# Performance work log

Measured on AMD Instinct MI355X. Metric: run time of the kernel, lower is better.

The kernel has to match this reference:

```python
import jax, jax.numpy as jnp
import numpy as np

B=64; HW=14; E=2048; L=30; V=10000; EMB=512; AML=768; ADL=500
D=512+ADL   # decoder_dim + article_downlen = 1012
A=512+ADL   # attention_dim + article_downlen = 1012

def setup_inputs() -> dict:
    key = jax.random.key(0)
    ks = jax.random.split(key, 20)
    s = 0.02
    lin = lambda k, i, o: (jax.random.normal(k, (i, o), jnp.float32) * s)
    inp = {}
    inp['encoder_out'] = jax.random.normal(ks[0], (B, HW, HW, E), jnp.float32)
    inp['encoded_captions'] = jax.random.randint(ks[1], (B, L), 0, V)
    cl = jax.random.randint(ks[2], (B, 1), 2, L + 1)
    inp['caption_lengths'] = cl.at[0, 0].set(L)  # ensure max decode length == L-1
    inp['encoded_articles'] = jax.random.normal(ks[3], (B, 1, AML), jnp.float32)
    inp['article_lengths'] = jax.random.randint(ks[4], (B, 1), 1, AML)
    inp['blank_context'] = 0
    inp['E_emb'] = jax.random.uniform(ks[5], (V, EMB), jnp.float32, -0.1, 0.1)
    inp['W_par'] = lin(ks[6], AML, ADL); inp['b_par'] = jnp.zeros(ADL, jnp.float32)
    inp['W_enc'] = lin(ks[7], E, A);     inp['b_enc'] = jnp.zeros(A, jnp.float32)
    inp['W_dec'] = lin(ks[8], D, A);     inp['b_dec'] = jnp.zeros(A, jnp.float32)
    inp['W_full'] = lin(ks[9], A, 1);    inp['b_full'] = jnp.zeros(1, jnp.float32)
    inp['W_h'] = lin(ks[10], E + ADL, D); inp['b_h'] = jnp.zeros(D, jnp.float32)
    inp['W_c'] = lin(ks[11], E + ADL, D); inp['b_c'] = jnp.zeros(D, jnp.float32)
    inp['W_fb'] = lin(ks[12], D, E);      inp['b_fb'] = jnp.zeros(E, jnp.float32)
    inp['W_ih'] = lin(ks[13], EMB + E, 4 * D); inp['b_ih'] = jnp.zeros(4 * D, jnp.float32)
    inp['W_hh'] = lin(ks[14], D, 4 * D);       inp['b_hh'] = jnp.zeros(4 * D, jnp.float32)
    inp['W_fc'] = jax.random.uniform(ks[15], (D, V), jnp.float32, -0.1, 0.1)
    inp['b_fc'] = jnp.zeros(V, jnp.float32)
    return inp

def reference(encoder_out, encoded_captions, caption_lengths, encoded_articles,
              article_lengths, blank_context, E_emb, W_par, b_par, W_enc, b_enc,
              W_dec, b_dec, W_full, b_full, W_h, b_h, W_c, b_c, W_fb, b_fb,
              W_ih, b_ih, W_hh, b_hh, W_fc, b_fc):
    Bv = encoder_out.shape[0]
    enc = encoder_out.reshape(Bv, -1, encoder_out.shape[-1])  # (B, P, E)
    lens = caption_lengths[:, 0]
    sort_ind = jnp.argsort(-lens)
    lens = lens[sort_ind]
    enc = enc[sort_ind]
    caps = encoded_captions[sort_ind]
    arts = encoded_articles[sort_ind]
    emb = E_emb[caps]                                   # (B, L, EMB)
    context = (arts @ W_par + b_par)[:, 0, :]           # ParagraphEncoder -> (B, ADL)
    dec_in = jnp.concatenate([enc.mean(axis=1), context], axis=1)
    h0 = dec_in @ W_h + b_h
    c0 = dec_in @ W_c + b_c
    dlens = lens - 1
    att1 = enc @ W_enc + b_enc                          # loop-invariant, (B, P, A)
    T = emb.shape[1] - 1

    def step(carry, t):
        h, c = carry
        active = (dlens > t)[:, None]                   # prefix mask (sorted desc)
        att2 = h @ W_dec + b_dec
        scores = (jax.nn.relu(att1 + att2[:, None, :]) @ W_full)[..., 0] + b_full[0]
        alpha = jax.nn.softmax(scores, axis=1)          # (B, P)
        awe = jnp.einsum('bp,bpe->be', alpha, enc)
        awe = jax.nn.sigmoid(h @ W_fb + b_fb) * awe     # gated attention encoding
        x = jnp.concatenate([emb[:, t, :], awe], axis=1)
        gates = x @ W_ih + b_ih + h @ W_hh + b_hh       # torch LSTMCell, gate order i,f,g,o
        i, f, g, o = jnp.split(gates, 4, axis=1)
        c_new = jax.nn.sigmoid(f) * c + jax.nn.sigmoid(i) * jnp.tanh(g)
        h_new = jax.nn.sigmoid(o) * jnp.tanh(c_new)
        preds = jnp.where(active, h_new @ W_fc + b_fc, 0.0)
        alpha_m = jnp.where(active, alpha, 0.0)
        h = jnp.where(active, h_new, h)
        c = jnp.where(active, c_new, c)
        return (h, c), (preds, alpha_m)

    _, (preds, alphas) = jax.lax.scan(step, (h0, c0), jnp.arange(T))
    predictions = jnp.transpose(preds, (1, 0, 2))       # (B, T, V)
    alphas = jnp.transpose(alphas, (1, 0, 2))           # (B, T, P)
    return (predictions, caps, dlens, alphas, sort_ind)
```

## Files before the change

kernel.cpp:

```cpp
#include <hip/hip_runtime.h>
#include <math.h>

#define B_   64
#define P_   196
#define E_   2048
#define L_   30
#define T_   29
#define V_   10000
#define EMB_ 512
#define AML_ 768
#define ADL_ 500
#define D_   1012
#define A_   1012
#define G4_  4048
#define XK_  2560

typedef unsigned short u16;
typedef __attribute__((ext_vector_type(8))) short bf16x8;
typedef __attribute__((ext_vector_type(4))) float f32x4;

__device__ __forceinline__ float sigf(float x) { return 1.f / (1.f + __expf(-x)); }
__device__ __forceinline__ float tanhf_fast(float x) { return 1.f - 2.f / (__expf(2.f * x) + 1.f); }
__device__ __forceinline__ u16 f2bf(float f) {
    unsigned u = __float_as_uint(f);
    return (u16)((u + 0x7FFFu + ((u >> 16) & 1u)) >> 16);
}
__device__ __forceinline__ float bf2f(u16 v) { return __uint_as_float(((unsigned)v) << 16); }

__global__ void k_setup(const int* __restrict__ clen, const int* __restrict__ caps,
                        float* __restrict__ out_caps, float* __restrict__ out_dlens,
                        float* __restrict__ out_sind,
                        int* __restrict__ sort_ind, int* __restrict__ dlens_i,
                        int* __restrict__ nact, int* __restrict__ caps_s)
{
    __shared__ int lens[B_];
    int t = threadIdx.x;
    if (t < B_) lens[t] = clen[t];
    __syncthreads();
    if (t < B_) {
        int my = lens[t];
        int rank = 0;
        for (int j = 0; j < B_; ++j) {
            int lj = lens[j];
            if (lj > my || (lj == my && j < t)) rank++;
        }
        sort_ind[rank] = t;
    }
    __syncthreads();
    if (t < B_) {
        int orig = sort_ind[t];
        int dl = lens[orig] - 1;
        dlens_i[t] = dl;
        out_dlens[t] = (float)dl;
        out_sind[t] = (float)orig;
        for (int j = 0; j < L_; ++j) {
            int cv = caps[orig * L_ + j];
            caps_s[t * L_ + j] = cv;
            out_caps[t * L_ + j] = (float)cv;
        }
    }
    __syncthreads();
    if (t < T_) {
        int cnt = 0;
        for (int j = 0; j < B_; ++j) cnt += (dlens_i[j] > t) ? 1 : 0;
        nact[t] = cnt;
    }
}

__global__ void k_zero(float4* __restrict__ p, long n4)
{
// ... 137 lines not shown
    const u16* w1p = W1 + (long)nc * K1 + lk;
    for (int k = 0; k < K1; k += 32) {
        bf16x8 bw = *(const bf16x8*)(w1p + k);
#pragma unroll
        for (int m = 0; m < 4; ++m)
            if (m < mmax) {
                bf16x8 aw = *(const bf16x8*)(a1p + (long)m * 16 * K1 + k);
                acc[m] = __builtin_amdgcn_mfma_f32_16x16x32_bf16(aw, bw, acc[m], 0, 0, 0);
            }
    }
    float bv = (n < Nmax) ? bias1[n] : 0.f;
#pragma unroll
    for (int m = 0; m < 4; ++m) {
        if (m < mmax) {
#pragma unroll
            for (int j = 0; j < 4; ++j) {
                int b = m * 16 + (lane >> 4) * 4 + j;
                if (b < Bact) {
                    float v = acc[m][j] + bv;
                    if (ACT == 1) v = sigf(v);
                    if (n < Nmax) {
                        if (OUT == 1) ((u16*)Yv)[(long)b * ldY + offY + n] = f2bf(v);
                        else          ((float*)Yv)[(long)b * ldY + offY + n] = v;
                    } else if (PADZ) {
                        if (OUT == 1) ((u16*)Yv)[(long)b * ldY + offY + n] = 0;
                        else          ((float*)Yv)[(long)b * ldY + offY + n] = 0.f;
                    }
                }
            }
        }
    }
}

__global__ void __launch_bounds__(256) k_att2fb(
    const u16* __restrict__ h_bf, const u16* __restrict__ WT_dec,
    const u16* __restrict__ WT_fb, const float* __restrict__ b_dec,
    const float* __restrict__ b_fb, float* __restrict__ att2p,
    float* __restrict__ fbp, const int* __restrict__ nact, int t)
{
    int Bact = nact[t];
    if (Bact <= 0) return;
    int mmax = (Bact + 15) >> 4;
    int kh = blockIdx.x >= 48;
    int nb = blockIdx.x - (kh ? 48 : 0);
    int isfb = nb >= 16;
    const u16* W = isfb ? WT_fb : WT_dec;
    const float* bias = isfb ? b_fb : b_dec;
    int Nmax = isfb ? E_ : A_;
    int nb2 = isfb ? nb - 16 : nb;
    long ldY = isfb ? (long)E_ : 1024L;
    float* Y = (isfb ? fbp : att2p) + (long)kh * B_ * ldY;

    int w = threadIdx.x >> 6, lane = threadIdx.x & 63;
    int lr = lane & 15, lk = (lane >> 4) * 8;
    int n = nb2 * 64 + w * 16 + lr;
    int nc = n < Nmax ? n : Nmax - 1;
    int k0 = kh * 512;
    f32x4 acc[4];
#pragma unroll
    for (int m = 0; m < 4; ++m) acc[m] = (f32x4){0.f, 0.f, 0.f, 0.f};
    const u16* ap = h_bf + (long)lr * 1024 + k0 + lk;
    const u16* wp = W + (long)nc * 1024 + k0 + lk;
    for (int k = 0; k < 512; k += 32) {
        bf16x8 bw = *(const bf16x8*)(wp + k);
#pragma unroll
        for (int m = 0; m < 4; ++m)
            if (m < mmax) {
                bf16x8 aw = *(const bf16x8*)(ap + (long)m * 16 * 1024 + k);
                acc[m] = __builtin_amdgcn_mfma_f32_16x16x32_bf16(aw, bw, acc[m], 0, 0, 0);
            }
    }
    if (n >= Nmax) return;
    float bv = (kh == 0) ? bias[n] : 0.f;
#pragma unroll
    for (int m = 0; m < 4; ++m) {
        if (m < mmax) {
#pragma unroll
            for (int j = 0; j < 4; ++j) {
                int b = m * 16 + (lane >> 4) * 4 + j;
                if (b < Bact) Y[(long)b * ldY + n] = acc[m][j] + bv;
            }
        }
    }
}

__global__ void k_scores(const u16* __restrict__ att1, const float* __restrict__ att2p,
                         const float* __restrict__ W_full, const float* __restrict__ b_full,
                         float* __restrict__ scores, const int* __restrict__ nact, int t)
{
    int b = blockIdx.y;
    if (b >= nact[t]) return;
    int wv = threadIdx.x >> 6;
    int lane = threadIdx.x & 63;
    int p = blockIdx.x * 4 + wv;
    const u16* a1 = att1 + ((long)b * P_ + p) * 1024;
    const float* a20 = att2p + (long)b * 1024;
    const float* a21 = att2p + (long)B_ * 1024 + (long)b * 1024;
    float acc = 0.f;
    for (int j2 = lane; j2 < 506; j2 += 64) {
        unsigned pk = *(const unsigned*)(a1 + 2 * j2);
        float2 p0 = *(const float2*)(a20 + 2 * j2);
        float2 p1 = *(const float2*)(a21 + 2 * j2);
        float2 wv2 = *(const float2*)(W_full + 2 * j2);
        float v0 = bf2f((u16)(pk & 0xFFFF)) + p0.x + p1.x;
        float v1 = bf2f((u16)(pk >> 16)) + p0.y + p1.y;
        v0 = v0 > 0.f ? v0 : 0.f;
        v1 = v1 > 0.f ? v1 : 0.f;
        acc = fmaf(v0, wv2.x, acc);
        acc = fmaf(v1, wv2.y, acc);
    }
    for (int m = 32; m >= 1; m >>= 1) acc += __shfl_xor(acc, m);
    if (lane == 0) scores[b * P_ + p] = acc + b_full[0];
}

__global__ void __launch_bounds__(256) k_awe_x(
    const u16* __restrict__ A_bf, const float* __restrict__ scores,
    const float* __restrict__ fbp, u16* __restrict__ awe_buf,
    float* __restrict__ alphas_out, const int* __restrict__ nact, int t)
{
    int b = blockIdx.y;
    if (b >= nact[t]) return;
    int tid = threadIdx.x;
    int w = tid >> 6, lane = tid & 63;
    __shared__ float al[P_];
    __shared__ float red[4];
    float v = (tid < P_) ? scores[b * P_ + tid] : -1e30f;
    float m = v;
    for (int s = 32; s >= 1; s >>= 1) m = fmaxf(m, __shfl_xor(m, s));
    if (lane == 0) red[w] = m;
    __syncthreads();
    m = fmaxf(fmaxf(red[0], red[1]), fmaxf(red[2], red[3]));
    float e = (tid < P_) ? __expf(v - m) : 0.f;
    float s_ = e;
    for (int s = 32; s >= 1; s >>= 1) s_ += __shfl_xor(s_, s);
    __syncthreads();
    if (lane == 0) red[w] = s_;
    __syncthreads();
    s_ = red[0] + red[1] + red[2] + red[3];
    if (tid < P_) al[tid] = e / s_;
    __syncthreads();

    if (blockIdx.x < 8) {
        int e0 = blockIdx.x * 256 + tid;
        const u16* src = A_bf + (long)b * P_ * E_ + e0;
        float s0 = 0.f, s1 = 0.f, s2 = 0.f, s3 = 0.f;
        for (int p = 0; p < P_; p += 4) {
            s0 = fmaf(al[p],     bf2f(src[(long)p * E_]), s0);
            s1 = fmaf(al[p + 1], bf2f(src[(long)(p + 1) * E_]), s1);
            s2 = fmaf(al[p + 2], bf2f(src[(long)(p + 2) * E_]), s2);
            s3 = fmaf(al[p + 3], bf2f(src[(long)(p + 3) * E_]), s3);
        }
        float g = sigf(fbp[(long)b * E_ + e0] + fbp[(long)(B_ + b) * E_ + e0]);
        awe_buf[(long)b * E_ + e0] = f2bf((s0 + s1 + s2 + s3) * g);
    } else {
        if (tid < P_) alphas_out[((long)b * T_ + t) * P_ + tid] = al[tid];
    }
}

__global__ void __launch_bounds__(256) k_gates(
    const u16* __restrict__ emb_t, const u16* __restrict__ awe,
    const u16* __restrict__ h_old, const u16* __restrict__ WT_ih,
    const u16* __restrict__ WT_hh, float* __restrict__ gpart,
    const int* __restrict__ nact, int t)
{
    int Bact = nact[t];
    if (Bact <= 0) return;
    int mmax = (Bact + 15) >> 4;
    int q = threadIdx.x >> 6;
    int lane = threadIdx.x & 63;
    int lr = lane & 15, lk = (lane >> 4) * 8;
    int kh = blockIdx.y;
    int n = blockIdx.x * 16 + lr;
    int nc = n < D_ ? n : D_ - 1;
    f32x4 acc[4];
#pragma unroll
    for (int m = 0; m < 4; ++m) acc[m] = (f32x4){0.f, 0.f, 0.f, 0.f};
    const u16* wih = WT_ih + ((long)q * D_ + nc) * XK_;
    const u16* whh = WT_hh + ((long)q * D_ + nc) * 1024;

    if (kh == 0) {
        const u16* ap = emb_t + (long)lr * EMB_ + lk;
        for (int k = 0; k < EMB_; k += 32) {
            bf16x8 bw = *(const bf16x8*)(wih + k);
#pragma unroll
            for (int m = 0; m < 4; ++m)
                if (m < mmax) {
                    bf16x8 aw = *(const bf16x8*)(ap + (long)m * 16 * EMB_ + k);
                    acc[m] = __builtin_amdgcn_mfma_f32_16x16x32_bf16(aw, bw, acc[m], 0, 0, 0);
                }
        }
        const u16* ap2 = awe + (long)lr * E_ + lk;
        const u16* w2 = wih + EMB_;
        for (int k = 0; k < 1280; k += 32) {
            bf16x8 bw = *(const bf16x8*)(w2 + k);
#pragma unroll
            for (int m = 0; m < 4; ++m)
                if (m < mmax) {
                    bf16x8 aw = *(const bf16x8*)(ap2 + (long)m * 16 * E_ + k);
                    acc[m] = __builtin_amdgcn_mfma_f32_16x16x32_bf16(aw, bw, acc[m], 0, 0, 0);
                }
        }
    } else {
        const u16* ap2 = awe + (long)lr * E_ + 1280 + lk;
        const u16* w2 = wih + 1792;
        for (int k = 0; k < 768; k += 32) {
            bf16x8 bw = *(const bf16x8*)(w2 + k);
#pragma unroll
            for (int m = 0; m < 4; ++m)
                if (m < mmax) {
                    bf16x8 aw = *(const bf16x8*)(ap2 + (long)m * 16 * E_ + k);
                    acc[m] = __builtin_amdgcn_mfma_f32_16x16x32_bf16(aw, bw, acc[m], 0, 0, 0);
                }
        }
        const u16* ap3 = h_old + (long)lr * 1024 + lk;
        for (int k = 0; k < 1024; k += 32) {
            bf16x8 bw = *(const bf16x8*)(whh + k);
#pragma unroll
            for (int m = 0; m < 4; ++m)
                if (m < mmax) {
                    bf16x8 aw = *(const bf16x8*)(ap3 + (long)m * 16 * 1024 + k);
                    acc[m] = __builtin_amdgcn_mfma_f32_16x16x32_bf16(aw, bw, acc[m], 0, 0, 0);
                }
        }
    }
#pragma unroll
    for (int m = 0; m < 4; ++m) {
        if (m < mmax) {
#pragma unroll
            for (int j = 0; j < 4; ++j) {
                int bb = m * 16 + (lane >> 4) * 4 + j;
                if (bb < Bact)
                    gpart[((long)kh * B_ + bb) * 4096 + q * 1024 + n] = acc[m][j];
            }
        }
    }
}

__global__ void k_lstm_red(const float* __restrict__ gpart, const float* __restrict__ b_ih,
                           const float* __restrict__ b_hh, float* __restrict__ cbuf,
                           u16* __restrict__ h_new, const int* __restrict__ nact, int t)
{
    int b = blockIdx.y;
    if (b >= nact[t]) return;
    int n = blockIdx.x * 256 + threadIdx.x;
    if (n >= D_) return;
    const float* g0 = gpart + (long)b * 4096;
    const float* g1 = gpart + (long)(B_ + b) * 4096;
    float gi = g0[n]        + g1[n]        + b_ih[n]          + b_hh[n];
    float gf = g0[1024 + n] + g1[1024 + n] + b_ih[D_ + n]     + b_hh[D_ + n];
    float gg = g0[2048 + n] + g1[2048 + n] + b_ih[2 * D_ + n] + b_hh[2 * D_ + n];
    float go = g0[3072 + n] + g1[3072 + n] + b_ih[3 * D_ + n] + b_hh[3 * D_ + n];
    float c = cbuf[(long)b * 1024 + n];
    float cn = sigf(gf) * c + sigf(gi) * tanhf_fast(gg);
    float hn = sigf(go) * tanhf_fast(cn);
    cbuf[(long)b * 1024 + n] = cn;
    h_new[(long)b * 1024 + n] = f2bf(hn);
}

__global__ void __launch_bounds__(256) k_fc_all(
    const u16* __restrict__ h_all, const u16* __restrict__ W,
    const float* __restrict__ bias, float* __restrict__ out_preds,
    const int* __restrict__ nact)
{
    int tslot = blockIdx.y;
    int Bact = nact[tslot];
    if (Bact <= 0) return;
    int mmax = (Bact + 15) >> 4;
    int w = threadIdx.x >> 6, lane = threadIdx.x & 63;
    int lr = lane & 15, lk = (lane >> 4) * 8;
    int n0 = blockIdx.x * 256 + w * 64;
    f32x4 acc[4][4];
#pragma unroll
    for (int i = 0; i < 4; ++i)
#pragma unroll
        for (int j = 0; j < 4; ++j) acc[i][j] = (f32x4){0.f, 0.f, 0.f, 0.f};
    const u16* ap = h_all + ((long)(tslot + 1) * B_ + lr) * 1024 + lk;
    int ncl[4];
#pragma unroll
    for (int nt = 0; nt < 4; ++nt) {
        int n = n0 + nt * 16 + lr;
        ncl[nt] = n < V_ ? n : V_ - 1;
    }
    for (int k = 0; k < 1024; k += 32) {
        bf16x8 af[4], bf[4];
#pragma unroll
        for (int mt = 0; mt < 4; ++mt)
            if (mt < mmax) af[mt] = *(const bf16x8*)(ap + (long)mt * 16 * 1024 + k);
#pragma unroll
        for (int nt = 0; nt < 4; ++nt) bf[nt] = *(const bf16x8*)(W + (long)ncl[nt] * 1024 + lk + k);
// ... 33 lines not shown
    const float* arts   = (const float*)d_in[3];
    const float* E_emb  = (const float*)d_in[6];
    const float* W_par  = (const float*)d_in[7];
    const float* b_par  = (const float*)d_in[8];
    const float* W_enc  = (const float*)d_in[9];
    const float* b_enc  = (const float*)d_in[10];
    const float* W_dec  = (const float*)d_in[11];
    const float* b_dec  = (const float*)d_in[12];
    const float* W_full = (const float*)d_in[13];
    const float* b_full = (const float*)d_in[14];
    const float* W_h    = (const float*)d_in[15];
    const float* b_h    = (const float*)d_in[16];
    const float* W_c    = (const float*)d_in[17];
    const float* b_c    = (const float*)d_in[18];
    const float* W_fb   = (const float*)d_in[19];
    const float* b_fb   = (const float*)d_in[20];
    const float* W_ih   = (const float*)d_in[21];
    const float* b_ih   = (const float*)d_in[22];
    const float* W_hh   = (const float*)d_in[23];
    const float* b_hh   = (const float*)d_in[24];
    const float* W_fc   = (const float*)d_in[25];
    const float* b_fc   = (const float*)d_in[26];

    float* out = (float*)d_out;
    float* out_preds  = out;
    float* out_caps   = out + (long)B_ * T_ * V_;
    float* out_dlens  = out_caps + B_ * L_;
    float* out_alphas = out_dlens + B_;
    float* out_sind   = out_alphas + (long)B_ * T_ * P_;

    float* ws = (float*)d_ws;
    long o = 0;
    auto alloc = [&](long n) { long r = o; o += (n + 63) & ~63L; return r; };
    long o_ints   = alloc(2176);
    long o_decin  = alloc((long)B_ * XK_ / 2);
    long o_hall   = alloc((long)(T_ + 1) * B_ * 1024 / 2);
    long o_emball = alloc((long)T_ * B_ * EMB_ / 2);
    long o_awe    = alloc((long)B_ * E_ / 2);
    long o_c      = alloc((long)B_ * 1024);
    long o_att2p  = alloc((long)2 * B_ * 1024);
    long o_fbp    = alloc((long)2 * B_ * E_);
    long o_gpart  = alloc((long)2 * B_ * 4096);
    long o_scores = alloc((long)B_ * P_);
    long o_Abf    = alloc((long)12544 * E_ / 2);
    long o_att1   = alloc((long)12544 * 1024 / 2);
    long o_wtenc  = alloc((long)1024 * 2048 / 2);
    long o_wtdec  = alloc((long)1024 * 1024 / 2);
    long o_wtfb   = alloc((long)2048 * 1024 / 2);
    long o_wtih   = alloc((long)4096 * 2560 / 2);
    long o_wthh   = alloc((long)4096 * 1024 / 2);
    long o_wtfc   = alloc((long)10048 * 1024 / 2);

    int* sort_ind = (int*)(ws + o_ints);
    int* dlens_i  = sort_ind + 64;
    int* nact     = dlens_i + 64;
    int* caps_s   = nact + 32;
    u16*   dec_in  = (u16*)(ws + o_decin);
    u16*   h_all   = (u16*)(ws + o_hall);
    u16*   emb_all = (u16*)(ws + o_emball);
    u16*   awe_buf = (u16*)(ws + o_awe);
    float* cbuf   = ws + o_c;
    float* att2p  = ws + o_att2p;
    float* fbp    = ws + o_fbp;
    float* gpart  = ws + o_gpart;
    float* scores = ws + o_scores;
    u16*   A_bf   = (u16*)(ws + o_Abf);
    u16*   att1   = (u16*)(ws + o_att1);
    u16*   WT_enc = (u16*)(ws + o_wtenc);
    u16*   WT_dec = (u16*)(ws + o_wtdec);
    u16*   WT_fb  = (u16*)(ws + o_wtfb);
    u16*   WT_ih  = (u16*)(ws + o_wtih);
    u16*   WT_hh  = (u16*)(ws + o_wthh);
    u16*   WT_fc  = (u16*)(ws + o_wtfc);
    u16*   WT_h   = att1;
    u16*   WT_c   = att1 + (long)1024 * XK_;

    long n4 = ((long)B_ * T_ * V_ + B_ * L_ + B_ + (long)B_ * T_ * P_ + B_) / 4;
    k_zero<<<dim3((unsigned)((n4 + 255) / 256)), 256, 0, stream>>>((float4*)d_out, n4);
    k_setup<<<1, 64, 0, stream>>>(clen, caps, out_caps, out_dlens, out_sind,
                                  sort_ind, dlens_i, nact, caps_s);

    k_encmean<<<dim3(8, 64), 256, 0, stream>>>(enc, sort_ind, dec_in);
    k_ctx<<<dim3(2, 64), 256, 0, stream>>>(arts, W_par, b_par, sort_ind, dec_in);
    k_emb_all<<<dim3(T_, 64), 256, 0, stream>>>(E_emb, caps_s, emb_all);

    dim3 tb(32, 8);
    k_transpose<<<dim3(1024/32, 2560/32), tb, 0, stream>>>(W_h, WT_h, 2548, 1012, 2560, 1024);
    k_transpose<<<dim3(1024/32, 2560/32), tb, 0, stream>>>(W_c, WT_c, 2548, 1012, 2560, 1024);
    k_skinny<0,1,1><<<dim3(16), 256, 0, stream>>>(dec_in, WT_h, XK_, b_h, h_all, 1024L, 0L, D_,
                                                  nact, -1);
    k_skinny<0,0,1><<<dim3(16), 256, 0, stream>>>(dec_in, WT_c, XK_, b_c, cbuf, 1024L, 0L, D_,
                                                  nact, -1);

    k_transpose<<<dim3(1024/32, 2048/32), tb, 0, stream>>>(W_enc, WT_enc, 2048, 1012, 2048, 1024);
    k_transpose<<<dim3(1024/32, 1024/32), tb, 0, stream>>>(W_dec, WT_dec, 1012, 1012, 1024, 1024);
    k_transpose<<<dim3(2048/32, 1024/32), tb, 0, stream>>>(W_fb, WT_fb, 1012, 2048, 1024, 2048);
    k_transpose<<<dim3(4096/32, 2560/32), tb, 0, stream>>>(W_ih, WT_ih, 2560, 4048, 2560, 4096);
    k_transpose<<<dim3(4096/32, 1024/32), tb, 0, stream>>>(W_hh, WT_hh, 1012, 4048, 1024, 4096);
    k_transpose<<<dim3(10048/32, 1024/32), tb, 0, stream>>>(W_fc, WT_fc, 1012, 10000, 1024, 10048);

    k_cvt_enc<<<dim3(2, 12544), 256, 0, stream>>>(enc, sort_ind, A_bf);
    k_att1_mfma<<<dim3(4, 196), 256, 0, stream>>>(A_bf, WT_enc, b_enc, att1);

    for (int t = 0; t < T_; ++t) {
        const u16* h_old = h_all + (long)t * B_ * 1024;
        u16* h_new = h_all + (long)(t + 1) * B_ * 1024;
        const u16* emb_t = emb_all + (long)t * B_ * EMB_;
        k_att2fb<<<dim3(96), 256, 0, stream>>>(h_old, WT_dec, WT_fb, b_dec, b_fb,
                                               att2p, fbp, nact, t);
        k_scores<<<dim3(49, 64), 256, 0, stream>>>(att1, att2p, W_full, b_full, scores, nact, t);
        k_awe_x<<<dim3(9, 64), 256, 0, stream>>>(A_bf, scores, fbp, awe_buf,
                                                 out_alphas, nact, t);
        k_gates<<<dim3(64, 2), 256, 0, stream>>>(emb_t, awe_buf, h_old, WT_ih, WT_hh,
                                                 gpart, nact, t);
        k_lstm_red<<<dim3(4, 64), 256, 0, stream>>>(gpart, b_ih, b_hh, cbuf, h_new, nact, t);
    }
    k_fc_all<<<dim3(40, T_), 256, 0, stream>>>(h_all, WT_fc, b_fc, out_preds, nact);
}
```

Measured before the change: 3.111 ms.

## Fuse per-timestep decoder kernels into one persistent cooperative kernel with grid syncs

Replaces the five kernel launches per timestep (145 total) with a single cooperative kernel of 256 blocks that loops over timesteps and separates the phases with grid.sync. The h@W_hh product moves into the first phase alongside att2/fb, so it no longer sits on the critical path after the attention work. The input-to-hidden gates are split four ways across K to give more blocks work. This removes launch overhead and inter-kernel gaps, at the cost of grid-wide barriers and a fixed grid of 256 blocks that limits parallelism in the scores and awe phases.

New measurement: 7.037 ms. 2.26x slower.

```diff
diff --git a/kernel.cpp b/kernel.cpp
--- a/kernel.cpp
+++ b/kernel.cpp
@@ -1,5 +1,8 @@
 #include <hip/hip_runtime.h>
+#include <hip/hip_cooperative_groups.h>
 #include <math.h>
+
+namespace cg = cooperative_groups;
 
 #define B_   64
 #define P_   196
@@ -239,229 +242,212 @@
     }
 }
 
-__global__ void __launch_bounds__(256) k_att2fb(
-    const u16* __restrict__ h_bf, const u16* __restrict__ WT_dec,
-    const u16* __restrict__ WT_fb, const float* __restrict__ b_dec,
-    const float* __restrict__ b_fb, float* __restrict__ att2p,
-    float* __restrict__ fbp, const int* __restrict__ nact, int t)
-{
-    int Bact = nact[t];
-    if (Bact <= 0) return;
-    int mmax = (Bact + 15) >> 4;
-    int kh = blockIdx.x >= 48;
-    int nb = blockIdx.x - (kh ? 48 : 0);
-    int isfb = nb >= 16;
-    const u16* W = isfb ? WT_fb : WT_dec;
-    const float* bias = isfb ? b_fb : b_dec;
-    int Nmax = isfb ? E_ : A_;
-    int nb2 = isfb ? nb - 16 : nb;
-    long ldY = isfb ? (long)E_ : 1024L;
-    float* Y = (isfb ? fbp : att2p) + (long)kh * B_ * ldY;
-
-    int w = threadIdx.x >> 6, lane = threadIdx.x & 63;
-    int lr = lane & 15, lk = (lane >> 4) * 8;
-    int n = nb2 * 64 + w * 16 + lr;
-    int nc = n < Nmax ? n : Nmax - 1;
-    int k0 = kh * 512;
-    f32x4 acc[4];
-#pragma unroll
-    for (int m = 0; m < 4; ++m) acc[m] = (f32x4){0.f, 0.f, 0.f, 0.f};
-    const u16* ap = h_bf + (long)lr * 1024 + k0 + lk;
-    const u16* wp = W + (long)nc * 1024 + k0 + lk;
-    for (int k = 0; k < 512; k += 32) {
-        bf16x8 bw = *(const bf16x8*)(wp + k);
-#pragma unroll
-        for (int m = 0; m < 4; ++m)
-            if (m < mmax) {
-                bf16x8 aw = *(const bf16x8*)(ap + (long)m * 16 * 1024 + k);
-                acc[m] = __builtin_amdgcn_mfma_f32_16x16x32_bf16(aw, bw, acc[m], 0, 0, 0);
-            }
-    }
-    if (n >= Nmax) return;
-    float bv = (kh == 0) ? bias[n] : 0.f;
-#pragma unroll
-    for (int m = 0; m < 4; ++m) {
-        if (m < mmax) {
-#pragma unroll
-            for (int j = 0; j < 4; ++j) {
-                int b = m * 16 + (lane >> 4) * 4 + j;
-                if (b < Bact) Y[(long)b * ldY + n] = acc[m][j] + bv;
-            }
-        }
-    }
-}
-
-__global__ void k_scores(const u16* __restrict__ att1, const float* __restrict__ att2p,
-                         const float* __restrict__ W_full, const float* __restrict__ b_full,
-                         float* __restrict__ scores, const int* __restrict__ nact, int t)
-{
-    int b = blockIdx.y;
-    if (b >= nact[t]) return;
-    int wv = threadIdx.x >> 6;
-    int lane = threadIdx.x & 63;
-    int p = blockIdx.x * 4 + wv;
-    const u16* a1 = att1 + ((long)b * P_ + p) * 1024;
-    const float* a20 = att2p + (long)b * 1024;
-    const float* a21 = att2p + (long)B_ * 1024 + (long)b * 1024;
-    float acc = 0.f;
-    for (int j2 = lane; j2 < 506; j2 += 64) {
-        unsigned pk = *(const unsigned*)(a1 + 2 * j2);
-        float2 p0 = *(const float2*)(a20 + 2 * j2);
-        float2 p1 = *(const float2*)(a21 + 2 * j2);
-        float2 wv2 = *(const float2*)(W_full + 2 * j2);
-        float v0 = bf2f((u16)(pk & 0xFFFF)) + p0.x + p1.x;
-        float v1 = bf2f((u16)(pk >> 16)) + p0.y + p1.y;
-        v0 = v0 > 0.f ? v0 : 0.f;
-        v1 = v1 > 0.f ? v1 : 0.f;
-        acc = fmaf(v0, wv2.x, acc);
-        acc = fmaf(v1, wv2.y, acc);
-    }
-    for (int m = 32; m >= 1; m >>= 1) acc += __shfl_xor(acc, m);
-    if (lane == 0) scores[b * P_ + p] = acc + b_full[0];
-}
-
-__global__ void __launch_bounds__(256) k_awe_x(
-    const u16* __restrict__ A_bf, const float* __restrict__ scores,
-    const float* __restrict__ fbp, u16* __restrict__ awe_buf,
-    float* __restrict__ alphas_out, const int* __restrict__ nact, int t)
-{
-    int b = blockIdx.y;
-    if (b >= nact[t]) return;
+__global__ void __launch_bounds__(256) k_loop(
+    const u16* __restrict__ A_bf, const u16* __restrict__ att1,
+    const u16* __restrict__ emb_all,
+    const u16* __restrict__ WT_dec, const u16* __restrict__ WT_fb,
+    const u16* __restrict__ WT_hh, const u16* __restrict__ WT_ih,
+    const float* __restrict__ W_full, const float* __restrict__ b_full,
+    const float* __restrict__ b_dec, const float* __restrict__ b_fb,
+    const float* __restrict__ b_ih, const float* __restrict__ b_hh,
+    u16* __restrict__ h_all, float* __restrict__ cbuf,
+    float* __restrict__ att2p, float* __restrict__ fbp, float* __restrict__ ghp,
+    float* __restrict__ gpart, float* __restrict__ scores,
+    u16* __restrict__ awe_buf, float* __restrict__ alphas_out,
+    const int* __restrict__ nact)
+{
+    cg::grid_group grid = cg::this_grid();
+    int bid = blockIdx.x;
     int tid = threadIdx.x;
     int w = tid >> 6, lane = tid & 63;
+    int lr = lane & 15, lk = (lane >> 4) * 8;
     __shared__ float al[P_];
     __shared__ float red[4];
-    float v = (tid < P_) ? scores[b * P_ + tid] : -1e30f;
-    float m = v;
-    for (int s = 32; s >= 1; s >>= 1) m = fmaxf(m, __shfl_xor(m, s));
-    if (lane == 0) red[w] = m;
-    __syncthreads();
-    m = fmaxf(fmaxf(red[0], red[1]), fmaxf(red[2], red[3]));
-    float e = (tid < P_) ? __expf(v - m) : 0.f;
-    float s_ = e;
-    for (int s = 32; s >= 1; s >>= 1) s_ += __shfl_xor(s_, s);
-    __syncthreads();
-    if (lane == 0) red[w] = s_;
-    __syncthreads();
-    s_ = red[0] + red[1] + red[2] + red[3];
-    if (tid < P_) al[tid] = e / s_;
-    __syncthreads();
-
-    if (blockIdx.x < 8) {
-        int e0 = blockIdx.x * 256 + tid;
-        const u16* src = A_bf + (long)b * P_ * E_ + e0;
-        float s0 = 0.f, s1 = 0.f, s2 = 0.f, s3 = 0.f;
-        for (int p = 0; p < P_; p += 4) {
-            s0 = fmaf(al[p],     bf2f(src[(long)p * E_]), s0);
-            s1 = fmaf(al[p + 1], bf2f(src[(long)(p + 1) * E_]), s1);
-            s2 = fmaf(al[p + 2], bf2f(src[(long)(p + 2) * E_]), s2);
-            s3 = fmaf(al[p + 3], bf2f(src[(long)(p + 3) * E_]), s3);
-        }
-        float g = sigf(fbp[(long)b * E_ + e0] + fbp[(long)(B_ + b) * E_ + e0]);
-        awe_buf[(long)b * E_ + e0] = f2bf((s0 + s1 + s2 + s3) * g);
-    } else {
-        if (tid < P_) alphas_out[((long)b * T_ + t) * P_ + tid] = al[tid];
-    }
-}
-
-__global__ void __launch_bounds__(256) k_gates(
-    const u16* __restrict__ emb_t, const u16* __restrict__ awe,
-    const u16* __restrict__ h_old, const u16* __restrict__ WT_ih,
-    const u16* __restrict__ WT_hh, float* __restrict__ gpart,
-    const int* __restrict__ nact, int t)
-{
-    int Bact = nact[t];
-    if (Bact <= 0) return;
-    int mmax = (Bact + 15) >> 4;
-    int q = threadIdx.x >> 6;
-    int lane = threadIdx.x & 63;
-    int lr = lane & 15, lk = (lane >> 4) * 8;
-    int kh = blockIdx.y;
-    int n = blockIdx.x * 16 + lr;
-    int nc = n < D_ ? n : D_ - 1;
-    f32x4 acc[4];
-#pragma unroll
-    for (int m = 0; m < 4; ++m) acc[m] = (f32x4){0.f, 0.f, 0.f, 0.f};
-    const u16* wih = WT_ih + ((long)q * D_ + nc) * XK_;
-    const u16* whh = WT_hh + ((long)q * D_ + nc) * 1024;
-
-    if (kh == 0) {
-        const u16* ap = emb_t + (long)lr * EMB_ + lk;
-        for (int k = 0; k < EMB_; k += 32) {
-            bf16x8 bw = *(const bf16x8*)(wih + k);
-#pragma unroll
-            for (int m = 0; m < 4; ++m)
+
+    for (int t = 0; t < T_; ++t) {
+        int Bact = nact[t];
+        int mmax = (Bact + 15) >> 4;
+        const u16* h_old = h_all + (long)t * B_ * 1024;
+        u16* h_new = h_all + (long)(t + 1) * B_ * 1024;
+        const u16* emb_t = emb_all + (long)t * B_ * EMB_;
+
+        if (bid < 224) {
+            int u = bid, mode, kh, nloc0;
+            const u16* Wb; float* Y; long ldY;
+            if (u < 32)      { mode = 0; kh = u >> 4; nloc0 = (u & 15) * 64; Wb = WT_dec; Y = att2p + (long)kh * 65536;  ldY = 1024; }
+            else if (u < 96) { u -= 32; mode = 1; kh = u >> 5; nloc0 = (u & 31) * 64; Wb = WT_fb; Y = fbp + (long)kh * 131072; ldY = 2048; }
+            else             { u -= 96; mode = 2; kh = u >> 6; nloc0 = (u & 63) * 64; Wb = WT_hh; Y = ghp + (long)kh * 262144; ldY = 4096; }
+            int nloc = nloc0 + w * 16 + lr;
+            int wrow;
+            if (mode == 0)      wrow = nloc < A_ ? nloc : A_ - 1;
+            else if (mode == 1) wrow = nloc;
+            else { int q = nloc >> 10, d = nloc & 1023; wrow = q * D_ + (d < D_ ? d : D_ - 1); }
+            int k0 = kh * 512;
+            f32x4 acc[4];
+#pragma unroll
+            for (int m = 0; m < 4; ++m) acc[m] = (f32x4){0.f, 0.f, 0.f, 0.f};
+            const u16* ap = h_old + (long)lr * 1024 + k0 + lk;
+            const u16* wp = Wb + (long)wrow * 1024 + k0 + lk;
+            for (int k = 0; k < 512; k += 32) {
+                bf16x8 bw = *(const bf16x8*)(wp + k);
+#pragma unroll
+                for (int m = 0; m < 4; ++m)
+                    if (m < mmax) {
+                        bf16x8 aw = *(const bf16x8*)(ap + (long)m * 16 * 1024 + k);
+                        acc[m] = __builtin_amdgcn_mfma_f32_16x16x32_bf16(aw, bw, acc[m], 0, 0, 0);
+                    }
+            }
+            float bv = 0.f;
+            if (kh == 0) {
+                if (mode == 0) bv = (nloc < A_) ? b_dec[nloc] : 0.f;
+                else if (mode == 1) bv = b_fb[nloc];
+            }
+#pragma unroll
+            for (int m = 0; m < 4; ++m) {
                 if (m < mmax) {
-                    bf16x8 aw = *(const bf16x8*)(ap + (long)m * 16 * EMB_ + k);
-                    acc[m] = __builtin_amdgcn_mfma_f32_16x16x32_bf16(aw, bw, acc[m], 0, 0, 0);
+#pragma unroll
+                    for (int j = 0; j < 4; ++j) {
+                        int bb = m * 16 + (lane >> 4) * 4 + j;
+                        if (bb < Bact) Y[(long)bb * ldY + nloc] = acc[m][j] + bv;
+                    }
                 }
-        }
-        const u16* ap2 = awe + (long)lr * E_ + lk;
-        const u16* w2 = wih + EMB_;
-        for (int k = 0; k < 1280; k += 32) {
-            bf16x8 bw = *(const bf16x8*)(w2 + k);
-#pragma unroll
-            for (int m = 0; m < 4; ++m)
+            }
+        }
+        grid.sync();
+
+        {
+            int wave_id = bid * 4 + w;
+            float bf0 = b_full[0];
+            for (int pair = wave_id; pair < B_ * P_; pair += 1024) {
+                int b = pair / P_, p = pair - b * P_;
+                if (b >= Bact) continue;
+                const u16* a1 = att1 + ((long)b * P_ + p) * 1024;
+                const float* a20 = att2p + (long)b * 1024;
+                const float* a21 = att2p + 65536 + (long)b * 1024;
+                float acc = 0.f;
+                for (int j2 = lane; j2 < 506; j2 += 64) {
+                    unsigned pk = *(const unsigned*)(a1 + 2 * j2);
+                    float2 p0 = *(const float2*)(a20 + 2 * j2);
+                    float2 p1 = *(const float2*)(a21 + 2 * j2);
+                    float2 wv2 = *(const float2*)(W_full + 2 * j2);
+                    float v0 = bf2f((u16)(pk & 0xFFFF)) + p0.x + p1.x;
+                    float v1 = bf2f((u16)(pk >> 16)) + p0.y + p1.y;
+                    v0 = v0 > 0.f ? v0 : 0.f;
+                    v1 = v1 > 0.f ? v1 : 0.f;
+                    acc = fmaf(v0, wv2.x, acc);
+                    acc = fmaf(v1, wv2.y, acc);
+                }
+                for (int m = 32; m >= 1; m >>= 1) acc += __shfl_xor(acc, m);
+                if (lane == 0) scores[b * P_ + p] = acc + bf0;
+            }
+        }
+        grid.sync();
+
+        {
+            int b = bid & 63;
+            if (b < Bact) {
+                float v = (tid < P_) ? scores[b * P_ + tid] : -1e30f;
+                float m = v;
+                for (int s = 32; s >= 1; s >>= 1) m = fmaxf(m, __shfl_xor(m, s));
+                if (lane == 0) red[w] = m;
+                __syncthreads();
+                m = fmaxf(fmaxf(red[0], red[1]), fmaxf(red[2], red[3]));
+                float e = (tid < P_) ? __expf(v - m) : 0.f;
+                float s_ = e;
+                for (int s = 32; s >= 1; s >>= 1) s_ += __shfl_xor(s_, s);
+                __syncthreads();
+                if (lane == 0) red[w] = s_;
+                __syncthreads();
+                s_ = red[0] + red[1] + red[2] + red[3];
+                if (tid < P_) al[tid] = e / s_;
+                __syncthreads();
+
+                for (int part = bid >> 6; part < 9; part += 4) {
+                    if (part < 8) {
+                        int e0 = part * 256 + tid;
+                        const u16* src = A_bf + (long)b * P_ * E_ + e0;
+                        float s0 = 0.f, s1 = 0.f, s2 = 0.f, s3 = 0.f;
+                        for (int p = 0; p < P_; p += 4) {
+                            s0 = fmaf(al[p],     bf2f(src[(long)p * E_]), s0);
+                            s1 = fmaf(al[p + 1], bf2f(src[(long)(p + 1) * E_]), s1);
+                            s2 = fmaf(al[p + 2], bf2f(src[(long)(p + 2) * E_]), s2);
+                            s3 = fmaf(al[p + 3], bf2f(src[(long)(p + 3) * E_]), s3);
+                        }
+                        float g = sigf(fbp[(long)b * 2048 + e0] + fbp[131072 + (long)b * 2048 + e0]);
+                        awe_buf[(long)b * E_ + e0] = f2bf((s0 + s1 + s2 + s3) * g);
+                    } else {
+                        if (tid < P_) alphas_out[((long)b * T_ + t) * P_ + tid] = al[tid];
+                    }
+                }
+            }
+        }
+        grid.sync();
+
+        {
+            int nblk = bid & 63, kpart = bid >> 6;
+            int q = w;
+            int n = nblk * 16 + lr;
+            int nc = n < D_ ? n : D_ - 1;
+            const u16* wih = WT_ih + ((long)q * D_ + nc) * XK_;
+            f32x4 acc[4];
+#pragma unroll
+            for (int m = 0; m < 4; ++m) acc[m] = (f32x4){0.f, 0.f, 0.f, 0.f};
+            const u16* ap; long astr; const u16* wp; int K;
+            if (kpart == 0)      { ap = emb_t + (long)lr * EMB_ + lk;          astr = 16 * EMB_; wp = wih;        K = 512; }
+            else if (kpart == 1) { ap = awe_buf + (long)lr * E_ + lk;          astr = 16 * E_;   wp = wih + 512;  K = 704; }
+            else if (kpart == 2) { ap = awe_buf + (long)lr * E_ + 704 + lk;    astr = 16 * E_;   wp = wih + 1216; K = 672; }
+            else                 { ap = awe_buf + (long)lr * E_ + 1376 + lk;   astr = 16 * E_;   wp = wih + 1888; K = 672; }
+            for (int k = 0; k < K; k += 32) {
+                bf16x8 bw = *(const bf16x8*)(wp + k);
+#pragma unroll
+                for (int m = 0; m < 4; ++m)
+                    if (m < mmax) {
+                        bf16x8 aw = *(const bf16x8*)(ap + (long)m * astr + k);
+                        acc[m] = __builtin_amdgcn_mfma_f32_16x16x32_bf16(aw, bw, acc[m], 0, 0, 0);
+                    }
+            }
+#pragma unroll
+            for (int m = 0; m < 4; ++m) {
                 if (m < mmax) {
-                    bf16x8 aw = *(const bf16x8*)(ap2 + (long)m * 16 * E_ + k);
-                    acc[m] = __builtin_amdgcn_mfma_f32_16x16x32_bf16(aw, bw, acc[m], 0, 0, 0);
+#pragma unroll
+                    for (int j = 0; j < 4; ++j) {
+                        int bb = m * 16 + (lane >> 4) * 4 + j;
+                        if (bb < Bact)
+                            gpart[((long)kpart * B_ + bb) * 4096 + q * 1024 + n] = acc[m][j];
+                    }
                 }
-        }
-    } else {
-        const u16* ap2 = awe + (long)lr * E_ + 1280 + lk;
-        const u16* w2 = wih + 1792;
-        for (int k = 0; k < 768; k += 32) {
-            bf16x8 bw = *(const bf16x8*)(w2 + k);
-#pragma unroll
-            for (int m = 0; m < 4; ++m)
-                if (m < mmax) {
-                    bf16x8 aw = *(const bf16x8*)(ap2 + (long)m * 16 * E_ + k);
-                    acc[m] = __builtin_amdgcn_mfma_f32_16x16x32_bf16(aw, bw, acc[m], 0, 0, 0);
+            }
+        }
+        grid.sync();
+
+        {
+            int idx = bid * 256 + tid;
+            int b = idx >> 10, n = idx & 1023;
+            if (b < Bact) {
+                if (n < D_) {
+                    const float* gp = gpart + (long)b * 4096 + n;
+                    const float* gh0 = ghp + (long)b * 4096 + n;
+                    const float* gh1 = ghp + 262144 + (long)b * 4096 + n;
+                    float gi = gp[0]    + gp[262144]        + gp[524288]        + gp[786432]
+                             + gh0[0]   + gh1[0]            + b_ih[n]           + b_hh[n];
+                    float gf = gp[1024] + gp[262144 + 1024] + gp[524288 + 1024] + gp[786432 + 1024]
+                             + gh0[1024] + gh1[1024]        + b_ih[D_ + n]      + b_hh[D_ + n];
+                    float gg = gp[2048] + gp[262144 + 2048] + gp[524288 + 2048] + gp[786432 + 2048]
+                             + gh0[2048] + gh1[2048]        + b_ih[2 * D_ + n]  + b_hh[2 * D_ + n];
+                    float go = gp[3072] + gp[262144 + 3072] + gp[524288 + 3072] + gp[786432 + 3072]
+                             + gh0[3072] + gh1[3072]        + b_ih[3 * D_ + n]  + b_hh[3 * D_ + n];
+                    float c = cbuf[(long)b * 1024 + n];
+                    float cn = sigf(gf) * c + sigf(gi) * tanhf_fast(gg);
+                    float hn = sigf(go) * tanhf_fast(cn);
+                    cbuf[(long)b * 1024 + n] = cn;
+                    h_new[(long)b * 1024 + n] = f2bf(hn);
+                } else {
+                    h_new[(long)b * 1024 + n] = 0;
                 }
-        }
-        const u16* ap3 = h_old + (long)lr * 1024 + lk;
-        for (int k = 0; k < 1024; k += 32) {
-            bf16x8 bw = *(const bf16x8*)(whh + k);
-#pragma unroll
-            for (int m = 0; m < 4; ++m)
-                if (m < mmax) {
-                    bf16x8 aw = *(const bf16x8*)(ap3 + (long)m * 16 * 1024 + k);
-                    acc[m] = __builtin_amdgcn_mfma_f32_16x16x32_bf16(aw, bw, acc[m], 0, 0, 0);
-                }
-        }
-    }
-#pragma unroll
-    for (int m = 0; m < 4; ++m) {
-        if (m < mmax) {
-#pragma unroll
-            for (int j = 0; j < 4; ++j) {
-                int bb = m * 16 + (lane >> 4) * 4 + j;
-                if (bb < Bact)
-                    gpart[((long)kh * B_ + bb) * 4096 + q * 1024 + n] = acc[m][j];
-            }
-        }
-    }
-}
-
-__global__ void k_lstm_red(const float* __restrict__ gpart, const float* __restrict__ b_ih,
-                           const float* __restrict__ b_hh, float* __restrict__ cbuf,
-                           u16* __restrict__ h_new, const int* __restrict__ nact, int t)
-{
-    int b = blockIdx.y;
-    if (b >= nact[t]) return;
-    int n = blockIdx.x * 256 + threadIdx.x;
-    if (n >= D_) return;
-    const float* g0 = gpart + (long)b * 4096;
-    const float* g1 = gpart + (long)(B_ + b) * 4096;
-    float gi = g0[n]        + g1[n]        + b_ih[n]          + b_hh[n];
-    float gf = g0[1024 + n] + g1[1024 + n] + b_ih[D_ + n]     + b_hh[D_ + n];
-    float gg = g0[2048 + n] + g1[2048 + n] + b_ih[2 * D_ + n] + b_hh[2 * D_ + n];
-    float go = g0[3072 + n] + g1[3072 + n] + b_ih[3 * D_ + n] + b_hh[3 * D_ + n];
-    float c = cbuf[(long)b * 1024 + n];
-    float cn = sigf(gf) * c + sigf(gi) * tanhf_fast(gg);
-    float hn = sigf(go) * tanhf_fast(cn);
-    cbuf[(long)b * 1024 + n] = cn;
-    h_new[(long)b * 1024 + n] = f2bf(hn);
+            }
+        }
+        grid.sync();
+    }
 }
 
 __global__ void __launch_bounds__(256) k_fc_all(
@@ -568,8 +554,9 @@
     long o_awe    = alloc((long)B_ * E_ / 2);
     long o_c      = alloc((long)B_ * 1024);
     long o_att2p  = alloc((long)2 * B_ * 1024);
-    long o_fbp    = alloc((long)2 * B_ * E_);
-    long o_gpart  = alloc((long)2 * B_ * 4096);
+    long o_fbp    = alloc((long)2 * B_ * 2048);
+    long o_ghp    = alloc((long)2 * B_ * 4096);
+    long o_gpart  = alloc((long)4 * B_ * 4096);
     long o_scores = alloc((long)B_ * P_);
     long o_Abf    = alloc((long)12544 * E_ / 2);
     long o_att1   = alloc((long)12544 * 1024 / 2);
@@ -591,8 +578,9 @@
     float* cbuf   = ws + o_c;
     float* att2p  = ws + o_att2p;
     float* fbp    = ws + o_fbp;
+    float* ghp    = ws + o_ghp;
     float* gpart  = ws + o_gpart;
-    float* scores = ws + o_scores;
+    float* scoresp = ws + o_scores;
     u16*   A_bf   = (u16*)(ws + o_Abf);
     u16*   att1   = (u16*)(ws + o_att1);
     u16*   WT_enc = (u16*)(ws + o_wtenc);
@@ -631,18 +619,19 @@
     k_cvt_enc<<<dim3(2, 12544), 256, 0, stream>>>(enc, sort_ind, A_bf);
     k_att1_mfma<<<dim3(4, 196), 256, 0, stream>>>(A_bf, WT_enc, b_enc, att1);
 
-    for (int t = 0; t < T_; ++t) {
-        const u16* h_old = h_all + (long)t * B_ * 1024;
-        u16* h_new = h_all + (long)(t + 1) * B_ * 1024;
-        const u16* emb_t = emb_all + (long)t * B_ * EMB_;
-        k_att2fb<<<dim3(96), 256, 0, stream>>>(h_old, WT_dec, WT_fb, b_dec, b_fb,
-                                               att2p, fbp, nact, t);
-        k_scores<<<dim3(49, 64), 256, 0, stream>>>(att1, att2p, W_full, b_full, scores, nact, t);
-        k_awe_x<<<dim3(9, 64), 256, 0, stream>>>(A_bf, scores, fbp, awe_buf,
-                                                 out_alphas, nact, t);
-        k_gates<<<dim3(64, 2), 256, 0, stream>>>(emb_t, awe_buf, h_old, WT_ih, WT_hh,
-                                                 gpart, nact, t);
-        k_lstm_red<<<dim3(4, 64), 256, 0, stream>>>(gpart, b_ih, b_hh, cbuf, h_new, nact, t);
-    }
+    {
+        void* kargs[] = {
+            (void*)&A_bf, (void*)&att1, (void*)&emb_all,
+            (void*)&WT_dec, (void*)&WT_fb, (void*)&WT_hh, (void*)&WT_ih,
+            (void*)&W_full, (void*)&b_full, (void*)&b_dec, (void*)&b_fb,
+            (void*)&b_ih, (void*)&b_hh,
+            (void*)&h_all, (void*)&cbuf,
+            (void*)&att2p, (void*)&fbp, (void*)&ghp, (void*)&gpart,
+            (void*)&scoresp, (void*)&awe_buf, (void*)&out_alphas,
+            (void*)&nact
+        };
+        hipLaunchCooperativeKernel((void*)k_loop, dim3(256), dim3(256), kargs, 0, stream);
+    }
+
     k_fc_all<<<dim3(40, T_), 256, 0, stream>>>(h_all, WT_fc, b_fc, out_preds, nact);
 }
```

## Split recurrent GEMMs four ways along K and fuse LSTM reduction via last-block atomic

Applied to the files above, without the earlier changes.

The att2/fb GEMM and the LSTM gate GEMM are now split four ways along K instead of two, doubling the number of blocks in these latency-bound per-step kernels. Downstream consumers sum four partial buffers. The separate LSTM reduction kernel is removed: the last of the four K-part blocks for each column tile is found with an atomic counter and threadfence, and it applies the gate nonlinearities. This saves one launch per step and adds atomics, fences and extra partial-sum traffic.

After: 3.196 ms. +2.8%, slower.

```diff
diff --git a/kernel.cpp b/kernel.cpp
--- a/kernel.cpp
+++ b/kernel.cpp
@@ -31,11 +31,13 @@
                         float* __restrict__ out_caps, float* __restrict__ out_dlens,
                         float* __restrict__ out_sind,
                         int* __restrict__ sort_ind, int* __restrict__ dlens_i,
-                        int* __restrict__ nact, int* __restrict__ caps_s)
+                        int* __restrict__ nact, int* __restrict__ caps_s,
+                        int* __restrict__ gcnt)
 {
     __shared__ int lens[B_];
     int t = threadIdx.x;
     if (t < B_) lens[t] = clen[t];
+    if (t < 64) gcnt[t] = 0;
     __syncthreads();
     if (t < B_) {
         int my = lens[t];
@@ -248,8 +250,8 @@
     int Bact = nact[t];
     if (Bact <= 0) return;
     int mmax = (Bact + 15) >> 4;
-    int kh = blockIdx.x >= 48;
-    int nb = blockIdx.x - (kh ? 48 : 0);
+    int kh = blockIdx.x / 48;
+    int nb = blockIdx.x - kh * 48;
     int isfb = nb >= 16;
     const u16* W = isfb ? WT_fb : WT_dec;
     const float* bias = isfb ? b_fb : b_dec;
@@ -262,13 +264,13 @@
     int lr = lane & 15, lk = (lane >> 4) * 8;
     int n = nb2 * 64 + w * 16 + lr;
     int nc = n < Nmax ? n : Nmax - 1;
-    int k0 = kh * 512;
+    int k0 = kh * 256;
     f32x4 acc[4];
 #pragma unroll
     for (int m = 0; m < 4; ++m) acc[m] = (f32x4){0.f, 0.f, 0.f, 0.f};
     const u16* ap = h_bf + (long)lr * 1024 + k0 + lk;
     const u16* wp = W + (long)nc * 1024 + k0 + lk;
-    for (int k = 0; k < 512; k += 32) {
+    for (int k = 0; k < 256; k += 32) {
         bf16x8 bw = *(const bf16x8*)(wp + k);
 #pragma unroll
         for (int m = 0; m < 4; ++m)
@@ -302,15 +304,19 @@
     int p = blockIdx.x * 4 + wv;
     const u16* a1 = att1 + ((long)b * P_ + p) * 1024;
     const float* a20 = att2p + (long)b * 1024;
-    const float* a21 = att2p + (long)B_ * 1024 + (long)b * 1024;
+    const float* a21 = a20 + 65536;
+    const float* a22 = a20 + 131072;
+    const float* a23 = a20 + 196608;
     float acc = 0.f;
     for (int j2 = lane; j2 < 506; j2 += 64) {
         unsigned pk = *(const unsigned*)(a1 + 2 * j2);
         float2 p0 = *(const float2*)(a20 + 2 * j2);
         float2 p1 = *(const float2*)(a21 + 2 * j2);
+        float2 p2 = *(const float2*)(a22 + 2 * j2);
+        float2 p3 = *(const float2*)(a23 + 2 * j2);
         float2 wv2 = *(const float2*)(W_full + 2 * j2);
-        float v0 = bf2f((u16)(pk & 0xFFFF)) + p0.x + p1.x;
-        float v1 = bf2f((u16)(pk >> 16)) + p0.y + p1.y;
+        float v0 = bf2f((u16)(pk & 0xFFFF)) + p0.x + p1.x + p2.x + p3.x;
+        float v1 = bf2f((u16)(pk >> 16)) + p0.y + p1.y + p2.y + p3.y;
         v0 = v0 > 0.f ? v0 : 0.f;
         v1 = v1 > 0.f ? v1 : 0.f;
         acc = fmaf(v0, wv2.x, acc);
@@ -357,17 +363,21 @@
             s2 = fmaf(al[p + 2], bf2f(src[(long)(p + 2) * E_]), s2);
             s3 = fmaf(al[p + 3], bf2f(src[(long)(p + 3) * E_]), s3);
         }
-        float g = sigf(fbp[(long)b * E_ + e0] + fbp[(long)(B_ + b) * E_ + e0]);
+        long fb_off = (long)b * E_ + e0;
+        float g = sigf(fbp[fb_off] + fbp[131072 + fb_off] + fbp[262144 + fb_off]
+                       + fbp[393216 + fb_off]);
         awe_buf[(long)b * E_ + e0] = f2bf((s0 + s1 + s2 + s3) * g);
     } else {
         if (tid < P_) alphas_out[((long)b * T_ + t) * P_ + tid] = al[tid];
     }
 }
 
-__global__ void __launch_bounds__(256) k_gates(
+__global__ void __launch_bounds__(256) k_gates_lstm3(
     const u16* __restrict__ emb_t, const u16* __restrict__ awe,
     const u16* __restrict__ h_old, const u16* __restrict__ WT_ih,
-    const u16* __restrict__ WT_hh, float* __restrict__ gpart,
+    const u16* __restrict__ WT_hh, const float* __restrict__ b_ih,
+    const float* __restrict__ b_hh, float* __restrict__ gpart,
+    int* __restrict__ gcnt, float* __restrict__ cbuf, u16* __restrict__ h_new,
     const int* __restrict__ nact, int t)
 {
     int Bact = nact[t];
@@ -376,8 +386,8 @@
     int q = threadIdx.x >> 6;
     int lane = threadIdx.x & 63;
     int lr = lane & 15, lk = (lane >> 4) * 8;
-    int kh = blockIdx.y;
-    int n = blockIdx.x * 16 + lr;
+    int nblk = blockIdx.x, kpart = blockIdx.y;
+    int n = nblk * 16 + lr;
     int nc = n < D_ ? n : D_ - 1;
     f32x4 acc[4];
 #pragma unroll
@@ -385,50 +395,19 @@
     const u16* wih = WT_ih + ((long)q * D_ + nc) * XK_;
     const u16* whh = WT_hh + ((long)q * D_ + nc) * 1024;
 
-    if (kh == 0) {
-        const u16* ap = emb_t + (long)lr * EMB_ + lk;
-        for (int k = 0; k < EMB_; k += 32) {
-            bf16x8 bw = *(const bf16x8*)(wih + k);
-#pragma unroll
-            for (int m = 0; m < 4; ++m)
-                if (m < mmax) {
-                    bf16x8 aw = *(const bf16x8*)(ap + (long)m * 16 * EMB_ + k);
-                    acc[m] = __builtin_amdgcn_mfma_f32_16x16x32_bf16(aw, bw, acc[m], 0, 0, 0);
-                }
-        }
-        const u16* ap2 = awe + (long)lr * E_ + lk;
-        const u16* w2 = wih + EMB_;
-        for (int k = 0; k < 1280; k += 32) {
-            bf16x8 bw = *(const bf16x8*)(w2 + k);
-#pragma unroll
-            for (int m = 0; m < 4; ++m)
-                if (m < mmax) {
-                    bf16x8 aw = *(const bf16x8*)(ap2 + (long)m * 16 * E_ + k);
-                    acc[m] = __builtin_amdgcn_mfma_f32_16x16x32_bf16(aw, bw, acc[m], 0, 0, 0);
-                }
-        }
-    } else {
-        const u16* ap2 = awe + (long)lr * E_ + 1280 + lk;
-        const u16* w2 = wih + 1792;
-        for (int k = 0; k < 768; k += 32) {
-            bf16x8 bw = *(const bf16x8*)(w2 + k);
-#pragma unroll
-            for (int m = 0; m < 4; ++m)
-                if (m < mmax) {
-                    bf16x8 aw = *(const bf16x8*)(ap2 + (long)m * 16 * E_ + k);
-                    acc[m] = __builtin_amdgcn_mfma_f32_16x16x32_bf16(aw, bw, acc[m], 0, 0, 0);
-                }
-        }
-        const u16* ap3 = h_old + (long)lr * 1024 + lk;
-        for (int k = 0; k < 1024; k += 32) {
-            bf16x8 bw = *(const bf16x8*)(whh + k);
-#pragma unroll
-            for (int m = 0; m < 4; ++m)
-                if (m < mmax) {
-                    bf16x8 aw = *(const bf16x8*)(ap3 + (long)m * 16 * 1024 + k);
-                    acc[m] = __builtin_amdgcn_mfma_f32_16x16x32_bf16(aw, bw, acc[m], 0, 0, 0);
-                }
-        }
+    const u16* ap; long astr; const u16* wp; int K;
+    if (kpart == 0)      { ap = emb_t + (long)lr * EMB_ + lk;        astr = 16 * EMB_; wp = wih;        K = 512; }
+    else if (kpart == 1) { ap = awe + (long)lr * E_ + lk;            astr = 16 * E_;   wp = wih + 512;  K = 1024; }
+    else if (kpart == 2) { ap = awe + (long)lr * E_ + 1024 + lk;     astr = 16 * E_;   wp = wih + 1536; K = 1024; }
+    else                 { ap = h_old + (long)lr * 1024 + lk;        astr = 16 * 1024; wp = whh;        K = 1024; }
+    for (int k = 0; k < K; k += 32) {
+        bf16x8 bw = *(const bf16x8*)(wp + k);
+#pragma unroll
+        for (int m = 0; m < 4; ++m)
+            if (m < mmax) {
+                bf16x8 aw = *(const bf16x8*)(ap + (long)m * astr + k);
+                acc[m] = __builtin_amdgcn_mfma_f32_16x16x32_bf16(aw, bw, acc[m], 0, 0, 0);
+            }
     }
 #pragma unroll
     for (int m = 0; m < 4; ++m) {
@@ -437,31 +416,40 @@
             for (int j = 0; j < 4; ++j) {
                 int bb = m * 16 + (lane >> 4) * 4 + j;
                 if (bb < Bact)
-                    gpart[((long)kh * B_ + bb) * 4096 + q * 1024 + n] = acc[m][j];
-            }
-        }
-    }
-}
-
-__global__ void k_lstm_red(const float* __restrict__ gpart, const float* __restrict__ b_ih,
-                           const float* __restrict__ b_hh, float* __restrict__ cbuf,
-                           u16* __restrict__ h_new, const int* __restrict__ nact, int t)
-{
-    int b = blockIdx.y;
-    if (b >= nact[t]) return;
-    int n = blockIdx.x * 256 + threadIdx.x;
-    if (n >= D_) return;
-    const float* g0 = gpart + (long)b * 4096;
-    const float* g1 = gpart + (long)(B_ + b) * 4096;
-    float gi = g0[n]        + g1[n]        + b_ih[n]          + b_hh[n];
-    float gf = g0[1024 + n] + g1[1024 + n] + b_ih[D_ + n]     + b_hh[D_ + n];
-    float gg = g0[2048 + n] + g1[2048 + n] + b_ih[2 * D_ + n] + b_hh[2 * D_ + n];
-    float go = g0[3072 + n] + g1[3072 + n] + b_ih[3 * D_ + n] + b_hh[3 * D_ + n];
-    float c = cbuf[(long)b * 1024 + n];
-    float cn = sigf(gf) * c + sigf(gi) * tanhf_fast(gg);
-    float hn = sigf(go) * tanhf_fast(cn);
-    cbuf[(long)b * 1024 + n] = cn;
-    h_new[(long)b * 1024 + n] = f2bf(hn);
+                    gpart[((long)kpart * B_ + bb) * 4096 + q * 1024 + n] = acc[m][j];
+            }
+        }
+    }
+    __threadfence();
+    __syncthreads();
+    __shared__ int isLast;
+    if (threadIdx.x == 0) isLast = (atomicAdd(&gcnt[nblk], 1) == 3) ? 1 : 0;
+    __syncthreads();
+    if (!isLast) return;
+    __threadfence();
+#pragma unroll
+    for (int i = 0; i < 4; ++i) {
+        int idx = threadIdx.x + i * 256;
+        int bb = idx >> 4, col = idx & 15;
+        if (bb >= Bact) continue;
+        int n2 = nblk * 16 + col;
+        if (n2 >= D_) continue;
+        const float* gp = gpart + (long)bb * 4096 + n2;
+        float gi = gp[0]    + gp[262144]        + gp[524288]        + gp[786432]
+                 + b_ih[n2]          + b_hh[n2];
+        float gf = gp[1024] + gp[262144 + 1024] + gp[524288 + 1024] + gp[786432 + 1024]
+                 + b_ih[D_ + n2]     + b_hh[D_ + n2];
+        float gg = gp[2048] + gp[262144 + 2048] + gp[524288 + 2048] + gp[786432 + 2048]
+                 + b_ih[2 * D_ + n2] + b_hh[2 * D_ + n2];
+        float go = gp[3072] + gp[262144 + 3072] + gp[524288 + 3072] + gp[786432 + 3072]
+                 + b_ih[3 * D_ + n2] + b_hh[3 * D_ + n2];
+        float c = cbuf[(long)bb * 1024 + n2];
+        float cn = sigf(gf) * c + sigf(gi) * tanhf_fast(gg);
+        float hn = sigf(go) * tanhf_fast(cn);
+        cbuf[(long)bb * 1024 + n2] = cn;
+        h_new[(long)bb * 1024 + n2] = f2bf(hn);
+    }
+    if (threadIdx.x == 0) atomicExch(&gcnt[nblk], 0);
 }
 
 __global__ void __launch_bounds__(256) k_fc_all(
@@ -561,15 +549,15 @@
     float* ws = (float*)d_ws;
     long o = 0;
     auto alloc = [&](long n) { long r = o; o += (n + 63) & ~63L; return r; };
-    long o_ints   = alloc(2176);
+    long o_ints   = alloc(2240);
     long o_decin  = alloc((long)B_ * XK_ / 2);
     long o_hall   = alloc((long)(T_ + 1) * B_ * 1024 / 2);
     long o_emball = alloc((long)T_ * B_ * EMB_ / 2);
     long o_awe    = alloc((long)B_ * E_ / 2);
     long o_c      = alloc((long)B_ * 1024);
-    long o_att2p  = alloc((long)2 * B_ * 1024);
-    long o_fbp    = alloc((long)2 * B_ * E_);
-    long o_gpart  = alloc((long)2 * B_ * 4096);
+    long o_att2p  = alloc((long)4 * B_ * 1024);
+    long o_fbp    = alloc((long)4 * B_ * 2048);
+    long o_gpart  = alloc((long)4 * B_ * 4096);
     long o_scores = alloc((long)B_ * P_);
     long o_Abf    = alloc((long)12544 * E_ / 2);
     long o_att1   = alloc((long)12544 * 1024 / 2);
@@ -584,6 +572,7 @@
     int* dlens_i  = sort_ind + 64;
     int* nact     = dlens_i + 64;
     int* caps_s   = nact + 32;
+    int* gcnt     = caps_s + B_ * L_;
     u16*   dec_in  = (u16*)(ws + o_decin);
     u16*   h_all   = (u16*)(ws + o_hall);
     u16*   emb_all = (u16*)(ws + o_emball);
@@ -607,7 +596,7 @@
     long n4 = ((long)B_ * T_ * V_ + B_ * L_ + B_ + (long)B_ * T_ * P_ + B_) / 4;
     k_zero<<<dim3((unsigned)((n4 + 255) / 256)), 256, 0, stream>>>((float4*)d_out, n4);
     k_setup<<<1, 64, 0, stream>>>(clen, caps, out_caps, out_dlens, out_sind,
-                                  sort_ind, dlens_i, nact, caps_s);
+                                  sort_ind, dlens_i, nact, caps_s, gcnt);
 
     k_encmean<<<dim3(8, 64), 256, 0, stream>>>(enc, sort_ind, dec_in);
     k_ctx<<<dim3(2, 64), 256, 0, stream>>>(arts, W_par, b_par, sort_ind, dec_in);
@@ -635,14 +624,14 @@
         const u16* h_old = h_all + (long)t * B_ * 1024;
         u16* h_new = h_all + (long)(t + 1) * B_ * 1024;
         const u16* emb_t = emb_all + (long)t * B_ * EMB_;
-        k_att2fb<<<dim3(96), 256, 0, stream>>>(h_old, WT_dec, WT_fb, b_dec, b_fb,
-                                               att2p, fbp, nact, t);
+        k_att2fb<<<dim3(192), 256, 0, stream>>>(h_old, WT_dec, WT_fb, b_dec, b_fb,
+                                                att2p, fbp, nact, t);
         k_scores<<<dim3(49, 64), 256, 0, stream>>>(att1, att2p, W_full, b_full, scores, nact, t);
         k_awe_x<<<dim3(9, 64), 256, 0, stream>>>(A_bf, scores, fbp, awe_buf,
                                                  out_alphas, nact, t);
-        k_gates<<<dim3(64, 2), 256, 0, stream>>>(emb_t, awe_buf, h_old, WT_ih, WT_hh,
-                                                 gpart, nact, t);
-        k_lstm_red<<<dim3(4, 64), 256, 0, stream>>>(gpart, b_ih, b_hh, cbuf, h_new, nact, t);
+        k_gates_lstm3<<<dim3(64, 4), 256, 0, stream>>>(emb_t, awe_buf, h_old, WT_ih, WT_hh,
+                                                       b_ih, b_hh, gpart, gcnt, cbuf, h_new,
+                                                       nact, t);
     }
     k_fc_all<<<dim3(40, T_), 256, 0, stream>>>(h_all, WT_fc, b_fc, out_preds, nact);
 }
```
